# Kernel tuning notes

Measured on AMD Instinct MI355X. Metric: run time of the kernel, lower is better.

Reference implementation:

```python
import jax, jax.numpy as jnp
import numpy as np

H = 256        # hidden_dim == num_features
C = 10         # num_classes
N = 100000     # nodes
E = 1600000    # edges
BN_EPS = 1e-5
NEG_SLOPE = 0.1


def _bn(h, gamma, beta):
    # training-mode BatchNorm1d over node dim, biased variance (torch semantics)
    mu = jnp.mean(h, axis=0)
    var = jnp.mean(jnp.square(h - mu), axis=0)
    return (h - mu) * jax.lax.rsqrt(var + BN_EPS) * gamma + beta


def setup_inputs() -> dict:
    key = jax.random.key(0)
    ks = jax.random.split(key, 12)
    s = 1.0 / np.sqrt(H)
    x = jax.random.normal(ks[0], (N, H), dtype=jnp.float32)
    edge_index = jax.random.randint(ks[1], (2, E), 0, N, dtype=jnp.int64)
    return {
        "x": x,
        "edge_index": edge_index,
        # GIN MLP: lin1 -> bn -> relu -> lin2
        "W1": jax.random.uniform(ks[2], (H, H), jnp.float32, -s, s),
        "b1": jnp.zeros((H,), jnp.float32),
        "g_mlp": jnp.ones((H,), jnp.float32),
        "be_mlp": jnp.zeros((H,), jnp.float32),
        "W2": jax.random.uniform(ks[3], (H, H), jnp.float32, -s, s),
        "b2": jnp.zeros((H,), jnp.float32),
        # bn4
        "g4": jnp.ones((H,), jnp.float32),
        "be4": jnp.zeros((H,), jnp.float32),
        # head
        "Wl1": jax.random.uniform(ks[4], (H, H // 2), jnp.float32, -s, s),
        "bl1": jnp.zeros((H // 2,), jnp.float32),
        "Wl3": jax.random.uniform(ks[5], (H // 2, C), jnp.float32, -s, s),
        "bl3": jnp.zeros((C,), jnp.float32),
    }


def reference(x, edge_index, W1, b1, g_mlp, be_mlp, W2, b2, g4, be4, Wl1, bl1, Wl3, bl3):
    lrelu = lambda h: jax.nn.leaky_relu(h, NEG_SLOPE)
    src, dst = edge_index[0], edge_index[1]
    # GINConv: sum-aggregate neighbor messages (source_to_target), eps=0
    agg = jax.ops.segment_sum(x[src], dst, num_segments=x.shape[0])  # [N,H]
    h = agg + x  # (1+eps)*x + sum
    # PyG MLP([H,H,H]): lin -> batch_norm -> relu -> lin (plain last)
    h = jax.nn.relu(_bn(h @ W1 + b1, g_mlp, be_mlp)) @ W2 + b2
    x1 = lrelu(h)                     # relu(conv1(...), 0.1); dropout p=0
    h = lrelu(x1)                     # relu(x1, 0.1)
    h = lrelu(_bn(h, g4, be4))        # relu(bn4(x), 0.1); dropout p=0
    h = x + 0.01 * h                  # residual with original features
    h = lrelu(h @ Wl1 + bl1)
    return h @ Wl3 + bl3              # [N, C]
```

## Files before the change

kernel.cpp:

```cpp
#include <hip/hip_runtime.h>

constexpr int NN = 100000;
constexpr int NE = 1600000;
constexpr int NBUCK = 782;
constexpr int CGRID = 98;

typedef __attribute__((ext_vector_type(4))) float  f32x4;
typedef __attribute__((ext_vector_type(2))) float  f32x2;
typedef __attribute__((ext_vector_type(8))) short  bf16x8;

__device__ __forceinline__ float bf2f(unsigned short u) {
  union { unsigned int i; float f; } c;
  c.i = ((unsigned int)u) << 16;
  return c.f;
}
__device__ __forceinline__ short f2bf(float f) {
  union { float f; unsigned int i; } c; c.f = f;
  unsigned int i = c.i + 0x7fffu + ((c.i >> 16) & 1u);
  return (short)(i >> 16);
}
__device__ __forceinline__ unsigned char f2fp8(float f) {
  int w = __builtin_amdgcn_cvt_pk_fp8_f32(f, 0.f, 0, false);
  return (unsigned char)(w & 0xff);
}
__device__ __forceinline__ void up4(int wv, float* f) {
  f32x2 a = __builtin_amdgcn_cvt_pk_f32_fp8(wv, false);
  f32x2 b = __builtin_amdgcn_cvt_pk_f32_fp8(wv, true);
  f[0] = a[0]; f[1] = a[1]; f[2] = b[0]; f[3] = b[1];
}

__device__ __forceinline__ void gload16(const void* g, void* l) {
  __builtin_amdgcn_global_load_lds(
      (const __attribute__((address_space(1))) unsigned int*)g,
      (__attribute__((address_space(3))) unsigned int*)l, 16, 0, 0);
}

__global__ void k_detect(const int* __restrict__ ew, int* __restrict__ flag,
                         float* __restrict__ zst) {
  __shared__ int bad;
  if (threadIdx.x == 0) bad = 0;
  for (int i = threadIdx.x; i < 1024; i += 256) zst[i] = 0.f;
  __syncthreads();
  int nz = 0;
  for (int i = threadIdx.x; i < 2048; i += 256) nz |= ew[2 * i + 1];
  if (nz) atomicOr(&bad, 1);
  __syncthreads();
  if (threadIdx.x == 0) *flag = (bad == 0) ? 1 : 0;
}

__global__ void k_cvtW(const float* __restrict__ W1, const float* __restrict__ W2,
                       const float* __restrict__ Wl1, const float* __restrict__ Wl3,
                       unsigned char* __restrict__ W1T8, unsigned char* __restrict__ W2T8,
                       short* __restrict__ Wl1T, short* __restrict__ Wl3T) {
  int b = blockIdx.x, t = threadIdx.x;
  if (b < 256)       W1T8[b * 256 + t]       = f2fp8(W1[t * 256 + b]);
  else if (b < 512){ int n = b - 256; W2T8[n * 256 + t] = f2fp8(W2[t * 256 + n]); }
  else if (b < 640){ int n = b - 512; Wl1T[n * 256 + t] = f2bf(Wl1[t * 128 + n]); }
  else {
    if (t < 128) {
#pragma unroll
      for (int c = 0; c < 16; ++c)
        Wl3T[c * 128 + t] = (c < 10) ? f2bf(Wl3[t * 10 + c]) : (short)0;
    }
  }
}

__global__ void k_cvtX(const float* __restrict__ x, void* __restrict__ xq) {
  int c = blockIdx.x * 256 + threadIdx.x;
  float4 a = ((const float4*)x)[2 * (size_t)c];
  float4 b = ((const float4*)x)[2 * (size_t)c + 1];
  int p0 = 0, p1 = 0;
  p0 = __builtin_amdgcn_cvt_pk_fp8_f32(a.x, a.y, p0, false);
  p0 = __builtin_amdgcn_cvt_pk_fp8_f32(a.z, a.w, p0, true);
  p1 = __builtin_amdgcn_cvt_pk_fp8_f32(b.x, b.y, p1, false);
  p1 = __builtin_amdgcn_cvt_pk_fp8_f32(b.z, b.w, p1, true);
  ((int2*)xq)[c] = make_int2(p0, p1);
}

__global__ __launch_bounds__(1024) void k_count(const int* __restrict__ ew,
                                                const int* __restrict__ flag,
                                                int* __restrict__ cntmat) {
  __shared__ int lcnt[NBUCK];
  int m64 = *flag;
  int t = threadIdx.x;
  for (int i = t; i < NBUCK; i += 1024) lcnt[i] = 0;
  __syncthreads();
  int base = blockIdx.x * 16384;
#pragma unroll
  for (int u = 0; u < 16; u++) {
    int e = base + u * 1024 + t;
    if (e < NE) {
      int d = m64 ? ew[2 * (NE + e)] : ew[NE + e];
      atomicAdd(&lcnt[d >> 7], 1);
    }
  }
  __syncthreads();
  for (int i = t; i < NBUCK; i += 1024) cntmat[blockIdx.x * NBUCK + i] = lcnt[i];
}

__global__ __launch_bounds__(256) void k_cscan(int* __restrict__ cntmat,
                                               int* __restrict__ tot) {
  int wid = (blockIdx.x * 256 + threadIdx.x) >> 6;
  int lane = threadIdx.x & 63;
  if (wid >= NBUCK) return;
  int v0 = (lane < CGRID) ? cntmat[lane * NBUCK + wid] : 0;
  int v1 = (lane + 64 < CGRID) ? cntmat[(lane + 64) * NBUCK + wid] : 0;
  int s0 = v0;
#pragma unroll
  for (int o = 1; o < 64; o <<= 1) { int u = __shfl_up(s0, o); if (lane >= o) s0 += u; }
  int s1 = v1;
#pragma unroll
  for (int o = 1; o < 64; o <<= 1) { int u = __shfl_up(s1, o); if (lane >= o) s1 += u; }
  int t0 = __shfl(s0, 63);
  int t1 = __shfl(s1, 63);
  if (lane < CGRID) cntmat[lane * NBUCK + wid] = s0 - v0;
  if (lane + 64 < CGRID) cntmat[(lane + 64) * NBUCK + wid] = t0 + s1 - v1;
  if (lane == 0) tot[wid] = t0 + t1;
}

__global__ __launch_bounds__(1024) void k_bscan(const int* __restrict__ tot,
                                                int* __restrict__ bases,
                                                int* __restrict__ off_) {
  __shared__ int s[1024];
  int t = threadIdx.x;
  int v = (t < NBUCK) ? tot[t] : 0;
  s[t] = v; __syncthreads();
  for (int o = 1; o < 1024; o <<= 1) {
    int u = (t >= o) ? s[t - o] : 0;
    __syncthreads();
    s[t] += u;
    __syncthreads();
  }
  if (t < NBUCK) bases[t] = s[t] - v;
  if (t == 0) { bases[NBUCK] = NE; off_[NN] = NE; }
}

__global__ __launch_bounds__(1024) void k_scatter(const int* __restrict__ ew,
                                                  const int* __restrict__ flag,
                                                  const int* __restrict__ cntmat,
                                                  const int* __restrict__ bases,
                                                  int* __restrict__ pairs) {
  __shared__ int lcur[NBUCK];
  int m64 = *flag;
  int t = threadIdx.x;
  for (int i = t; i < NBUCK; i += 1024)
    lcur[i] = bases[i] + cntmat[blockIdx.x * NBUCK + i];
  __syncthreads();
  int base = blockIdx.x * 16384;
#pragma unroll
  for (int u = 0; u < 16; u++) {
    int e = base + u * 1024 + t;
    if (e < NE) {
      int d = m64 ? ew[2 * (NE + e)] : ew[NE + e];
      int s = m64 ? ew[2 * e] : ew[e];
      int slot = atomicAdd(&lcur[d >> 7], 1);
      pairs[slot] = s | ((d & 127) << 17);
    }
  }
}

__global__ __launch_bounds__(256) void k_bsort(const int* __restrict__ pairs,
                                               const int* __restrict__ bases,
                                               int* __restrict__ off_,
                                               int* __restrict__ csr) {
  __shared__ int lcnt[128], lofs[128], lcur[128];
  int b = blockIdx.x, t = threadIdx.x;
  int s0 = bases[b], s1 = bases[b + 1];
  if (t < 128) lcnt[t] = 0;
  __syncthreads();
  for (int j = s0 + t; j < s1; j += 256) atomicAdd(&lcnt[(pairs[j] >> 17) & 127], 1);
  __syncthreads();
  int v = (t < 128) ? lcnt[t] : 0;
  if (t < 128) lofs[t] = v;
  __syncthreads();
  for (int o = 1; o < 128; o <<= 1) {
    int u = (t >= o && t < 128) ? lofs[t - o] : 0;
    __syncthreads();
    if (t < 128) lofs[t] += u;
    __syncthreads();
  }
  if (t < 128) {
    int ex = lofs[t] - v;
    lcur[t] = ex;
    int node = b * 128 + t;
    if (node < NN) off_[node] = s0 + ex;
  }
  __syncthreads();
  for (int j = s0 + t; j < s1; j += 256) {
    int p = pairs[j];
    int slot = atomicAdd(&lcur[(p >> 17) & 127], 1);
    csr[s0 + slot] = p & 0x1FFFF;
  }
}

__global__ __launch_bounds__(256) void k_agg2(const void* __restrict__ xq,
                                              const int* __restrict__ off_,
                                              const int* __restrict__ csr,
                                              unsigned char* __restrict__ h0) {
  int node = blockIdx.x * 4 + (threadIdx.x >> 6);
  int lane = threadIdx.x & 63;
  const unsigned char* xb = (const unsigned char*)xq;
  size_t boff = (size_t)lane * 4;
  int s0 = off_[node], s1 = off_[node + 1];
  int sw = *(const int*)(xb + (size_t)node * 256 + boff);
  f32x2 slo = __builtin_amdgcn_cvt_pk_f32_fp8(sw, false);
  f32x2 shi = __builtin_amdgcn_cvt_pk_f32_fp8(sw, true);
  float a0 = slo[0], a1 = slo[1], a2 = shi[0], a3 = shi[1];
  int j = s0;
  while (j + 8 <= s1) {
    int idx[8];
#pragma unroll
    for (int u = 0; u < 8; u++) idx[u] = csr[j + u];
    int w[8];
#pragma unroll
    for (int u = 0; u < 8; u++) w[u] = *(const int*)(xb + (size_t)idx[u] * 256 + boff);
#pragma unroll
    for (int u = 0; u < 8; u++) {
      f32x2 lo = __builtin_amdgcn_cvt_pk_f32_fp8(w[u], false);
      f32x2 hi = __builtin_amdgcn_cvt_pk_f32_fp8(w[u], true);
      a0 += lo[0]; a1 += lo[1]; a2 += hi[0]; a3 += hi[1];
    }
    j += 8;
  }
  if (j + 4 <= s1) {
    int idx[4];
#pragma unroll
    for (int u = 0; u < 4; u++) idx[u] = csr[j + u];
    int w[4];
#pragma unroll
    for (int u = 0; u < 4; u++) w[u] = *(const int*)(xb + (size_t)idx[u] * 256 + boff);
#pragma unroll
    for (int u = 0; u < 4; u++) {
      f32x2 lo = __builtin_amdgcn_cvt_pk_f32_fp8(w[u], false);
      f32x2 hi = __builtin_amdgcn_cvt_pk_f32_fp8(w[u], true);
      a0 += lo[0]; a1 += lo[1]; a2 += hi[0]; a3 += hi[1];
    }
    j += 4;
  }
  for (; j < s1; j++) {
    int s = csr[j];
    int w = *(const int*)(xb + (size_t)s * 256 + boff);
    f32x2 lo = __builtin_amdgcn_cvt_pk_f32_fp8(w, false);
    f32x2 hi = __builtin_amdgcn_cvt_pk_f32_fp8(w, true);
    a0 += lo[0]; a1 += lo[1]; a2 += hi[0]; a3 += hi[1];
  }
  int o = 0;
  o = __builtin_amdgcn_cvt_pk_fp8_f32(a0, a1, o, false);
  o = __builtin_amdgcn_cvt_pk_fp8_f32(a2, a3, o, true);
  ((int*)h0)[(size_t)node * 64 + lane] = o;
}

template <int ACT, int TIN, int STATS>
__global__ __launch_bounds__(256, 2) void k_gemm8(
    const unsigned char* __restrict__ A, const unsigned char* __restrict__ BT,
    const float* __restrict__ bias, unsigned char* __restrict__ C, int M,
    const float* __restrict__ tsum, const float* __restrict__ tssq,
    const float* __restrict__ tg, const float* __restrict__ tbe,
    float* __restrict__ gsum, float* __restrict__ gssq) {
  __shared__ char smem[32768];
  __shared__ float lsc[256], lsh[256];
  __shared__ float lsum[128], lssq[128];
  int tid = threadIdx.x, lane = tid & 63, w = tid >> 6;
  if (TIN) {
    float mu = tsum[tid] / (float)M;
    float var = tssq[tid] / (float)M - mu * mu;
    float rs = rsqrtf(var + 1e-5f);
    float sc = tg[tid] * rs;
    lsc[tid] = sc; lsh[tid] = tbe[tid] - mu * sc;
  }
  if (STATS && tid < 128) { lsum[tid] = 0.f; lssq[tid] = 0.f; }
  int bm = blockIdx.x >> 1, bn = blockIdx.x & 1;
  int bm0 = bm * 128, bn0 = bn * 128;
  int wm = w >> 1, wn = w & 1;
  int lr = lane & 15, lg = lane >> 4;
  f32x4 acc[4][4] = {};
  __syncthreads();

  int4 stg[2];

#pragma unroll 1
  for (int it = 0; it < 4; ++it) {
    int b = it & 1;
    if (it == 0) {
      if (TIN) {
#pragma unroll
        for (int i = 0; i < 2; ++i) {
          int p = i * 256 + tid, unit = p >> 3, u = (p & 7) ^ (unit & 7);
          int srow = unit * 2 + (u >> 2), slot = u & 3;
          int grow = bm0 + srow; if (grow > M - 1) grow = M - 1;
          stg[i] = *(const int4*)(A + (size_t)grow * 256 + slot * 16);
        }
      } else {
#pragma unroll
        for (int q = 0; q < 2; ++q) {
          int wc = w * 2 + q;
          int p = wc * 64 + lane, unit = p >> 3, u = (p & 7) ^ (unit & 7);
          int srow = unit * 2 + (u >> 2), slot = u & 3;
          int grow = bm0 + srow; if (grow > M - 1) grow = M - 1;
          gload16(A + (size_t)grow * 256 + slot * 16, smem + wc * 1024);
        }
      }
#pragma unroll
      for (int q = 0; q < 2; ++q) {
        int wc = w * 2 + q;
        int p = wc * 64 + lane, unit = p >> 3, u = (p & 7) ^ (unit & 7);
        int srow = unit * 2 + (u >> 2), slot = u & 3;
        gload16(BT + (size_t)(bn0 + srow) * 256 + slot * 16, smem + 8192 + wc * 1024);
      }
      if (TIN) {
#pragma unroll
        for (int i = 0; i < 2; ++i) {
          int p = i * 256 + tid, unit = p >> 3, u = (p & 7) ^ (unit & 7);
          int slot = u & 3;
          int k0 = slot * 16;
          float f[16];
          up4(stg[i].x, f); up4(stg[i].y, f + 4); up4(stg[i].z, f + 8); up4(stg[i].w, f + 12);
#pragma unroll
          for (int jj = 0; jj < 16; ++jj) f[jj] = fmaxf(f[jj] * lsc[k0 + jj] + lsh[k0 + jj], 0.f);
          int w0 = 0, w1 = 0, w2 = 0, w3 = 0;
          w0 = __builtin_amdgcn_cvt_pk_fp8_f32(f[0], f[1], w0, false);
          w0 = __builtin_amdgcn_cvt_pk_fp8_f32(f[2], f[3], w0, true);
          w1 = __builtin_amdgcn_cvt_pk_fp8_f32(f[4], f[5], w1, false);
          w1 = __builtin_amdgcn_cvt_pk_fp8_f32(f[6], f[7], w1, true);
          w2 = __builtin_amdgcn_cvt_pk_fp8_f32(f[8], f[9], w2, false);
          w2 = __builtin_amdgcn_cvt_pk_fp8_f32(f[10], f[11], w2, true);
          w3 = __builtin_amdgcn_cvt_pk_fp8_f32(f[12], f[13], w3, false);
          w3 = __builtin_amdgcn_cvt_pk_fp8_f32(f[14], f[15], w3, true);
          *(int4*)(smem + p * 16) = make_int4(w0, w1, w2, w3);
        }
      }
      __syncthreads();
    }
    int ktn = (it + 1) * 64;
    if (it < 3) {
      char* nb = smem + (b ^ 1) * 16384;
      if (TIN) {
#pragma unroll
        for (int i = 0; i < 2; ++i) {
          int p = i * 256 + tid, unit = p >> 3, u = (p & 7) ^ (unit & 7);
          int srow = unit * 2 + (u >> 2), slot = u & 3;
          int grow = bm0 + srow; if (grow > M - 1) grow = M - 1;
          stg[i] = *(const int4*)(A + (size_t)grow * 256 + ktn + slot * 16);
        }
      } else {
#pragma unroll
        for (int q = 0; q < 2; ++q) {
          int wc = w * 2 + q;
          int p = wc * 64 + lane, unit = p >> 3, u = (p & 7) ^ (unit & 7);
          int srow = unit * 2 + (u >> 2), slot = u & 3;
          int grow = bm0 + srow; if (grow > M - 1) grow = M - 1;
          gload16(A + (size_t)grow * 256 + ktn + slot * 16, nb + wc * 1024);
        }
      }
#pragma unroll
      for (int q = 0; q < 2; ++q) {
        int wc = w * 2 + q;
        int p = wc * 64 + lane, unit = p >> 3, u = (p & 7) ^ (unit & 7);
        int srow = unit * 2 + (u >> 2), slot = u & 3;
        gload16(BT + (size_t)(bn0 + srow) * 256 + ktn + slot * 16, nb + 8192 + wc * 1024);
      }
    }
    const char* sa = smem + b * 16384;
    const char* sb = sa + 8192;
#pragma unroll
    for (int ks = 0; ks < 2; ++ks) {
      long af[4], bfr[4];
#pragma unroll
      for (int mi = 0; mi < 4; ++mi) {
        int row = wm * 64 + mi * 16 + lr;
        int unit = row >> 1;
        int u = ((row & 1) * 4 + ks * 2 + (lg >> 1)) ^ (unit & 7);
        af[mi] = *(const long*)(sa + unit * 128 + u * 16 + (lg & 1) * 8);
      }
#pragma unroll
      for (int ni = 0; ni < 4; ++ni) {
        int row = wn * 64 + ni * 16 + lr;
        int unit = row >> 1;
        int u = ((row & 1) * 4 + ks * 2 + (lg >> 1)) ^ (unit & 7);
        bfr[ni] = *(const long*)(sb + unit * 128 + u * 16 + (lg & 1) * 8);
      }
#pragma unroll
      for (int mi = 0; mi < 4; ++mi)
#pragma unroll
        for (int ni = 0; ni < 4; ++ni)
          acc[mi][ni] = __builtin_amdgcn_mfma_f32_16x16x32_fp8_fp8(af[mi], bfr[ni], acc[mi][ni], 0, 0, 0);
    }
    if (TIN && it < 3) {
      char* nb = smem + (b ^ 1) * 16384;
#pragma unroll
      for (int i = 0; i < 2; ++i) {
        int p = i * 256 + tid, unit = p >> 3, u = (p & 7) ^ (unit & 7);
        int slot = u & 3;
        int k0 = ktn + slot * 16;
        float f[16];
        up4(stg[i].x, f); up4(stg[i].y, f + 4); up4(stg[i].z, f + 8); up4(stg[i].w, f + 12);
#pragma unroll
        for (int jj = 0; jj < 16; ++jj) f[jj] = fmaxf(f[jj] * lsc[k0 + jj] + lsh[k0 + jj], 0.f);
        int w0 = 0, w1 = 0, w2 = 0, w3 = 0;
        w0 = __builtin_amdgcn_cvt_pk_fp8_f32(f[0], f[1], w0, false);
        w0 = __builtin_amdgcn_cvt_pk_fp8_f32(f[2], f[3], w0, true);
        w1 = __builtin_amdgcn_cvt_pk_fp8_f32(f[4], f[5], w1, false);
        w1 = __builtin_amdgcn_cvt_pk_fp8_f32(f[6], f[7], w1, true);
        w2 = __builtin_amdgcn_cvt_pk_fp8_f32(f[8], f[9], w2, false);
        w2 = __builtin_amdgcn_cvt_pk_fp8_f32(f[10], f[11], w2, true);
        w3 = __builtin_amdgcn_cvt_pk_fp8_f32(f[12], f[13], w3, false);
        w3 = __builtin_amdgcn_cvt_pk_fp8_f32(f[14], f[15], w3, true);
        *(int4*)(nb + p * 16) = make_int4(w0, w1, w2, w3);
      }
    }
    __syncthreads();
  }

  unsigned char* zs = (unsigned char*)smem;
#pragma unroll
  for (int ni = 0; ni < 4; ++ni) {
    int col = wn * 64 + ni * 16 + lr;
    float bv = bias[bn0 + col];
    float ps = 0.f, pq = 0.f;
#pragma unroll
    for (int mi = 0; mi < 4; ++mi) {
#pragma unroll
      for (int r = 0; r < 4; ++r) {
        int row = wm * 64 + mi * 16 + lg * 4 + r;
        float tv = acc[mi][ni][r] + bv;
        if (ACT == 1) tv = tv > 0.f ? tv : 0.01f * tv;
        if (STATS && (bm0 + row) < M) { ps += tv; pq += tv * tv; }
        zs[row * 144 + col] = f2fp8(tv);
      }
    }
    if (STATS) {
      ps += __shfl_xor(ps, 16); pq += __shfl_xor(pq, 16);
      ps += __shfl_xor(ps, 32); pq += __shfl_xor(pq, 32);
      if (lane < 16) {
        atomicAdd(&lsum[wn * 64 + ni * 16 + lane], ps);
        atomicAdd(&lssq[wn * 64 + ni * 16 + lane], pq);
      }
    }
  }
  __syncthreads();
  {
    int row = tid >> 1;
    int grow = bm0 + row;
    if (grow < M) {
#pragma unroll
      for (int i = 0; i < 4; ++i) {
        int cs = (tid & 1) * 64 + i * 16;
        int4 v = *(const int4*)(zs + row * 144 + cs);
        *(int4*)(C + (size_t)grow * 256 + bn0 + cs) = v;
      }
    }
  }
  if (STATS) {
    if (tid < 128) {
      atomicAdd(&gsum[bn0 + tid], lsum[tid]);
      atomicAdd(&gssq[bn0 + tid], lssq[tid]);
    }
  }
}

__global__ __launch_bounds__(256, 2) void k_head(const unsigned char* __restrict__ Vq,
                                                 const float* __restrict__ x,
                                                 const short* __restrict__ BT,
                                                 const float* __restrict__ bl1,
                                                 const short* __restrict__ wl3t,
                                                 const float* __restrict__ bl3,
                                                 const float* __restrict__ tsum,
                                                 const float* __restrict__ tssq,
                                                 const float* __restrict__ tg,
                                                 const float* __restrict__ tbe,
                                                 float* __restrict__ out, int M) {
  __shared__ char smem[65536];
  __shared__ float lsc[256], lsh[256];
  __shared__ short wl3s[2048];
  int tid = threadIdx.x;
  int lane = tid & 63, w = tid >> 6;
  {
    float mu = tsum[tid] / (float)M;
    float var = tssq[tid] / (float)M - mu * mu;
    float rs = rsqrtf(var + 1e-5f);
    float sc = tg[tid] * rs;
    lsc[tid] = sc; lsh[tid] = tbe[tid] - mu * sc;
  }
  {
    int p = w * 64 + lane;
    gload16(wl3t + (size_t)p * 8, (char*)wl3s + w * 1024);
  }
  int bm0 = blockIdx.x * 128;
  int wm = w >> 1, wn = w & 1;
  int lr = lane & 15, lg = lane >> 4;
  f32x4 acc[4][4] = {};
  __syncthreads();

  int2 stgv[4];
  float stgx[4][8];

#pragma unroll 1
  for (int it = 0; it < 4; ++it) {
    int b = it & 1;
    if (it == 0) {
#pragma unroll
      for (int i = 0; i < 4; ++i) {
        int p = tid + 256 * i, row = p >> 3, s = (p & 7) ^ (row & 7);
        int grow = bm0 + row; if (grow > M - 1) grow = M - 1;
        size_t base = (size_t)grow * 256 + s * 8;
        stgv[i] = *(const int2*)(Vq + base);
        *(float4*)&stgx[i][0] = *(const float4*)(x + base);
        *(float4*)&stgx[i][4] = *(const float4*)(x + base + 4);
      }
#pragma unroll
      for (int q = 0; q < 4; ++q) {
        int wc = w * 4 + q;
        int p = wc * 64 + lane, row = p >> 3, s = (p & 7) ^ (row & 7);
        gload16(BT + (size_t)row * 256 + s * 8, smem + 16384 + wc * 1024);
      }
#pragma unroll
      for (int i = 0; i < 4; ++i) {
        int p = tid + 256 * i, row = p >> 3, s = (p & 7) ^ (row & 7);
        int k0 = s * 8;
        float fv[8];
        up4(stgv[i].x, fv); up4(stgv[i].y, fv + 4);
        bf16x8 o;
#pragma unroll
        for (int jj = 0; jj < 8; ++jj) {
          float f = fv[jj] * lsc[k0 + jj] + lsh[k0 + jj];
          f = f > 0.f ? f : 0.1f * f;
          o[jj] = f2bf(stgx[i][jj] + 0.01f * f);
        }
        *(bf16x8*)(smem + p * 16) = o;
      }
      __syncthreads();
    }
    int ktn = (it + 1) * 64;
    if (it < 3) {
      char* nb = smem + (b ^ 1) * 32768;
#pragma unroll
      for (int i = 0; i < 4; ++i) {
        int p = tid + 256 * i, row = p >> 3, s = (p & 7) ^ (row & 7);
        int grow = bm0 + row; if (grow > M - 1) grow = M - 1;
        size_t base = (size_t)grow * 256 + ktn + s * 8;
        stgv[i] = *(const int2*)(Vq + base);
        *(float4*)&stgx[i][0] = *(const float4*)(x + base);
        *(float4*)&stgx[i][4] = *(const float4*)(x + base + 4);
      }
#pragma unroll
      for (int q = 0; q < 4; ++q) {
        int wc = w * 4 + q;
        int p = wc * 64 + lane, row = p >> 3, s = (p & 7) ^ (row & 7);
        gload16(BT + (size_t)row * 256 + ktn + s * 8, nb + 16384 + wc * 1024);
      }
    }
    const char* sa = smem + b * 32768;
    const char* sb = sa + 16384;
#pragma unroll
    for (int ks = 0; ks < 2; ++ks) {
      bf16x8 af[4], bfr[4];
#pragma unroll
      for (int mi = 0; mi < 4; ++mi) {
        int row = wm * 64 + mi * 16 + lr;
        int q = (lg + 4 * ks) ^ (row & 7);
        af[mi] = *(const bf16x8*)(sa + row * 128 + q * 16);
      }
#pragma unroll
      for (int ni = 0; ni < 4; ++ni) {
        int row = wn * 64 + ni * 16 + lr;
        int q = (lg + 4 * ks) ^ (row & 7);
        bfr[ni] = *(const bf16x8*)(sb + row * 128 + q * 16);
      }
#pragma unroll
      for (int mi = 0; mi < 4; ++mi)
#pragma unroll
        for (int ni = 0; ni < 4; ++ni)
          acc[mi][ni] = __builtin_amdgcn_mfma_f32_16x16x32_bf16(af[mi], bfr[ni], acc[mi][ni], 0, 0, 0);
    }
    if (it < 3) {
      char* nb = smem + (b ^ 1) * 32768;
#pragma unroll
      for (int i = 0; i < 4; ++i) {
        int p = tid + 256 * i, row = p >> 3, s = (p & 7) ^ (row & 7);
        int k0 = ktn + s * 8;
        float fv[8];
        up4(stgv[i].x, fv); up4(stgv[i].y, fv + 4);
        bf16x8 o;
#pragma unroll
        for (int jj = 0; jj < 8; ++jj) {
          float f = fv[jj] * lsc[k0 + jj] + lsh[k0 + jj];
          f = f > 0.f ? f : 0.1f * f;
          o[jj] = f2bf(stgx[i][jj] + 0.01f * f);
        }
        *(bf16x8*)(nb + p * 16) = o;
      }
    }
    __syncthreads();
  }

  short* zs = (short*)smem;
#pragma unroll
  for (int ni = 0; ni < 4; ++ni) {
    int col = wn * 64 + ni * 16 + lr;
    float bv = bl1[col];
#pragma unroll
    for (int mi = 0; mi < 4; ++mi) {
#pragma unroll
      for (int r = 0; r < 4; ++r) {
        int row = wm * 64 + mi * 16 + lg * 4 + r;
        float tv = acc[mi][ni][r] + bv;
        tv = tv > 0.f ? tv : 0.1f * tv;
        zs[row * 136 + col] = f2bf(tv);
      }
    }
  }
  __syncthreads();

  f32x4 acc2[2] = {};
#pragma unroll
  for (int kk = 0; kk < 4; ++kk) {
    bf16x8 bfr = *(const bf16x8*)((const char*)wl3s + lr * 256 + (kk * 4 + lg) * 16);
#pragma unroll
    for (int m = 0; m < 2; ++m) {
      int row = (w * 2 + m) * 16 + lr;
      bf16x8 af = *(const bf16x8*)((const char*)zs + row * 272 + (kk * 4 + lg) * 16);
      acc2[m] = __builtin_amdgcn_mfma_f32_16x16x32_bf16(af, bfr, acc2[m], 0, 0, 0);
    }
  }
  if (lr < 10) {
    float bv = bl3[lr];
#pragma unroll
    for (int m = 0; m < 2; ++m) {
#pragma unroll
      for (int r = 0; r < 4; ++r) {
        int row = (w * 2 + m) * 16 + lg * 4 + r;
        int grow = bm0 + row;
        if (grow < M) out[(size_t)grow * 10 + lr] = acc2[m][r] + bv;
      }
    }
  }
}

extern "C" void kernel_launch(void* const* d_in, const int* in_sizes, int n_in,
                              void* d_out, int out_size, void* d_ws, size_t ws_size,
                              hipStream_t stream) {
  const float* x   = (const float*)d_in[0];
  const int*   ew  = (const int*)d_in[1];
  const float* W1  = (const float*)d_in[2];
  const float* b1  = (const float*)d_in[3];
  const float* g1  = (const float*)d_in[4];
  const float* be1 = (const float*)d_in[5];
  const float* W2  = (const float*)d_in[6];
  const float* b2  = (const float*)d_in[7];
  const float* g4  = (const float*)d_in[8];
  const float* be4 = (const float*)d_in[9];
  const float* Wl1 = (const float*)d_in[10];
  const float* bl1 = (const float*)d_in[11];
  const float* Wl3 = (const float*)d_in[12];
  const float* bl3 = (const float*)d_in[13];
  float* out = (float*)d_out;

  char* ws = (char*)d_ws;
  const size_t OFF_OFF  = 0;
  const size_t OFF_BASES= 400128;
  const size_t OFF_CNT  = 800256;
  const size_t OFF_WL3T = 1106944;
  const size_t OFF_TOT  = 1114112;
  const size_t OFF_STATS= 1200384;
  const size_t OFF_FLAG = 1208576;
  const size_t OFF_W1T  = 1209216;
  const size_t OFF_W2T  = 1340288;
  const size_t OFF_WL1T = 1471360;
  const size_t OFF_CSR  = 1536896;
  const size_t OFF_BUFA = 7936896;
  const size_t OFF_BUFB = 59136896;
  if (ws_size < 110336896) return;

  int* off_  = (int*)(ws + OFF_OFF);
  int* bases_= (int*)(ws + OFF_BASES);
  int* cnt_  = (int*)(ws + OFF_CNT);
  int* tot_  = (int*)(ws + OFF_TOT);
  float* sum1 = (float*)(ws + OFF_STATS);
  float* ssq1 = sum1 + 256;
  float* sum4 = sum1 + 512;
  float* ssq4 = sum1 + 768;
  int* flag_ = (int*)(ws + OFF_FLAG);
  unsigned char* W1T8 = (unsigned char*)(ws + OFF_W1T);
  unsigned char* W2T8 = (unsigned char*)(ws + OFF_W2T);
  short* Wl1T = (short*)(ws + OFF_WL1T);
  short* Wl3T = (short*)(ws + OFF_WL3T);
  int* csr_   = (int*)(ws + OFF_CSR);
  unsigned char* bufA = (unsigned char*)(ws + OFF_BUFA);
  unsigned char* bufB = (unsigned char*)(ws + OFF_BUFB);
  int* pairs_ = (int*)(ws + OFF_BUFA);
  void* xq    = (void*)bufB;

  k_detect<<<1, 256, 0, stream>>>(ew, flag_, sum1);
  k_cvtW<<<641, 256, 0, stream>>>(W1, W2, Wl1, Wl3, W1T8, W2T8, Wl1T, Wl3T);
  k_cvtX<<<12500, 256, 0, stream>>>(x, xq);
  k_count<<<CGRID, 1024, 0, stream>>>(ew, flag_, cnt_);
  k_cscan<<<196, 256, 0, stream>>>(cnt_, tot_);
  k_bscan<<<1, 1024, 0, stream>>>(tot_, bases_, off_);
  k_scatter<<<CGRID, 1024, 0, stream>>>(ew, flag_, cnt_, bases_, pairs_);
  k_bsort<<<NBUCK, 256, 0, stream>>>(pairs_, bases_, off_, csr_);
  k_agg2<<<25000, 256, 0, stream>>>(xq, off_, csr_, bufA);
  k_gemm8<0, 0, 1><<<1564, 256, 0, stream>>>(bufA, W1T8, b1, bufB, NN,
                                             nullptr, nullptr, nullptr, nullptr,
                                             sum1, ssq1);
  k_gemm8<1, 1, 1><<<1564, 256, 0, stream>>>(bufB, W2T8, b2, bufA, NN,
                                             sum1, ssq1, g1, be1, sum4, ssq4);
  k_head<<<782, 256, 0, stream>>>(bufA, x, Wl1T, bl1, Wl3T, bl3,
                                  sum4, ssq4, g4, be4, out, NN);
}
```

Measured before the change: 257.6 us.

## Merge detect, weight convert, x convert and edge count into one phase kernel

Four independent preprocessing kernels (int64 detection, weight transpose/convert, x fp8 conversion, destination bucket counting) are combined into one launch that picks its role from the block index. Each block that needs the int64 flag now recomputes it locally instead of reading a flag from a separate kernel. This removes three kernel launches and their serialization gaps, and lets the small jobs overlap with the large x conversion. In exchange the edge-layout check is done redundantly in every count and scatter block, and the 1024-thread blocks may change occupancy for the conversion part.

```diff
diff --git a/kernel.cpp b/kernel.cpp
--- a/kernel.cpp
+++ b/kernel.cpp
@@ -4,6 +4,9 @@
 constexpr int NE = 1600000;
 constexpr int NBUCK = 782;
 constexpr int CGRID = 98;
+constexpr int PH_CVTX = 3125;
+constexpr int PH_CNT_END = PH_CVTX + CGRID;
+constexpr int PH_GRID = PH_CNT_END + 161;
 
 typedef __attribute__((ext_vector_type(4))) float  f32x4;
 typedef __attribute__((ext_vector_type(2))) float  f32x2;
@@ -35,67 +38,65 @@
       (__attribute__((address_space(3))) unsigned int*)l, 16, 0, 0);
 }
 
-__global__ void k_detect(const int* __restrict__ ew, int* __restrict__ flag,
-                         float* __restrict__ zst) {
-  __shared__ int bad;
-  if (threadIdx.x == 0) bad = 0;
-  for (int i = threadIdx.x; i < 1024; i += 256) zst[i] = 0.f;
-  __syncthreads();
-  int nz = 0;
-  for (int i = threadIdx.x; i < 2048; i += 256) nz |= ew[2 * i + 1];
-  if (nz) atomicOr(&bad, 1);
-  __syncthreads();
-  if (threadIdx.x == 0) *flag = (bad == 0) ? 1 : 0;
-}
-
-__global__ void k_cvtW(const float* __restrict__ W1, const float* __restrict__ W2,
-                       const float* __restrict__ Wl1, const float* __restrict__ Wl3,
-                       unsigned char* __restrict__ W1T8, unsigned char* __restrict__ W2T8,
-                       short* __restrict__ Wl1T, short* __restrict__ Wl3T) {
-  int b = blockIdx.x, t = threadIdx.x;
-  if (b < 256)       W1T8[b * 256 + t]       = f2fp8(W1[t * 256 + b]);
-  else if (b < 512){ int n = b - 256; W2T8[n * 256 + t] = f2fp8(W2[t * 256 + n]); }
-  else if (b < 640){ int n = b - 512; Wl1T[n * 256 + t] = f2bf(Wl1[t * 128 + n]); }
-  else {
-    if (t < 128) {
-#pragma unroll
-      for (int c = 0; c < 16; ++c)
-        Wl3T[c * 128 + t] = (c < 10) ? f2bf(Wl3[t * 10 + c]) : (short)0;
-    }
-  }
-}
-
-__global__ void k_cvtX(const float* __restrict__ x, void* __restrict__ xq) {
-  int c = blockIdx.x * 256 + threadIdx.x;
-  float4 a = ((const float4*)x)[2 * (size_t)c];
-  float4 b = ((const float4*)x)[2 * (size_t)c + 1];
-  int p0 = 0, p1 = 0;
-  p0 = __builtin_amdgcn_cvt_pk_fp8_f32(a.x, a.y, p0, false);
-  p0 = __builtin_amdgcn_cvt_pk_fp8_f32(a.z, a.w, p0, true);
-  p1 = __builtin_amdgcn_cvt_pk_fp8_f32(b.x, b.y, p1, false);
-  p1 = __builtin_amdgcn_cvt_pk_fp8_f32(b.z, b.w, p1, true);
-  ((int2*)xq)[c] = make_int2(p0, p1);
-}
-
-__global__ __launch_bounds__(1024) void k_count(const int* __restrict__ ew,
-                                                const int* __restrict__ flag,
-                                                int* __restrict__ cntmat) {
+__global__ __launch_bounds__(1024) void k_phase1(
+    const float* __restrict__ x, void* __restrict__ xq,
+    const int* __restrict__ ew, int* __restrict__ cntmat,
+    const float* __restrict__ W1, const float* __restrict__ W2,
+    const float* __restrict__ Wl1, const float* __restrict__ Wl3,
+    unsigned char* __restrict__ W1T8, unsigned char* __restrict__ W2T8,
+    short* __restrict__ Wl1T, short* __restrict__ Wl3T,
+    float* __restrict__ zst) {
   __shared__ int lcnt[NBUCK];
-  int m64 = *flag;
-  int t = threadIdx.x;
-  for (int i = t; i < NBUCK; i += 1024) lcnt[i] = 0;
-  __syncthreads();
-  int base = blockIdx.x * 16384;
-#pragma unroll
-  for (int u = 0; u < 16; u++) {
-    int e = base + u * 1024 + t;
-    if (e < NE) {
-      int d = m64 ? ew[2 * (NE + e)] : ew[NE + e];
-      atomicAdd(&lcnt[d >> 7], 1);
-    }
-  }
-  __syncthreads();
-  for (int i = t; i < NBUCK; i += 1024) cntmat[blockIdx.x * NBUCK + i] = lcnt[i];
+  __shared__ int badsh;
+  int bid = blockIdx.x, tid = threadIdx.x;
+  if (bid < PH_CVTX) {
+    int c = bid * 1024 + tid;
+    float4 a = ((const float4*)x)[2 * (size_t)c];
+    float4 b = ((const float4*)x)[2 * (size_t)c + 1];
+    int p0 = 0, p1 = 0;
+    p0 = __builtin_amdgcn_cvt_pk_fp8_f32(a.x, a.y, p0, false);
+    p0 = __builtin_amdgcn_cvt_pk_fp8_f32(a.z, a.w, p0, true);
+    p1 = __builtin_amdgcn_cvt_pk_fp8_f32(b.x, b.y, p1, false);
+    p1 = __builtin_amdgcn_cvt_pk_fp8_f32(b.z, b.w, p1, true);
+    ((int2*)xq)[c] = make_int2(p0, p1);
+  } else if (bid < PH_CNT_END) {
+    int cb = bid - PH_CVTX;
+    if (tid == 0) badsh = 0;
+    for (int i = tid; i < NBUCK; i += 1024) lcnt[i] = 0;
+    __syncthreads();
+    int nz = 0;
+    for (int i = tid; i < 2048; i += 1024) nz |= ew[2 * i + 1];
+    if (nz) atomicOr(&badsh, 1);
+    __syncthreads();
+    int m64 = (badsh == 0);
+    int base = cb * 16384;
+#pragma unroll
+    for (int u = 0; u < 16; u++) {
+      int e = base + u * 1024 + tid;
+      if (e < NE) {
+        int d = m64 ? ew[2 * (NE + e)] : ew[NE + e];
+        atomicAdd(&lcnt[d >> 7], 1);
+      }
+    }
+    __syncthreads();
+    for (int i = tid; i < NBUCK; i += 1024) cntmat[cb * NBUCK + i] = lcnt[i];
+  } else {
+    int wb = bid - PH_CNT_END;
+    if (wb == 0) zst[tid] = 0.f;
+    int b = wb * 4 + (tid >> 8), t = tid & 255;
+    if (b < 641) {
+      if (b < 256)       W1T8[b * 256 + t]       = f2fp8(W1[t * 256 + b]);
+      else if (b < 512){ int n = b - 256; W2T8[n * 256 + t] = f2fp8(W2[t * 256 + n]); }
+      else if (b < 640){ int n = b - 512; Wl1T[n * 256 + t] = f2bf(Wl1[t * 128 + n]); }
+      else {
+        if (t < 128) {
+#pragma unroll
+          for (int c = 0; c < 16; ++c)
+            Wl3T[c * 128 + t] = (c < 10) ? f2bf(Wl3[t * 10 + c]) : (short)0;
+        }
+      }
+    }
+  }
 }
 
 __global__ __launch_bounds__(256) void k_cscan(int* __restrict__ cntmat,
@@ -136,16 +137,21 @@
 }
 
 __global__ __launch_bounds__(1024) void k_scatter(const int* __restrict__ ew,
-                                                  const int* __restrict__ flag,
                                                   const int* __restrict__ cntmat,
                                                   const int* __restrict__ bases,
                                                   int* __restrict__ pairs) {
   __shared__ int lcur[NBUCK];
-  int m64 = *flag;
+  __shared__ int badsh;
   int t = threadIdx.x;
+  if (t == 0) badsh = 0;
   for (int i = t; i < NBUCK; i += 1024)
     lcur[i] = bases[i] + cntmat[blockIdx.x * NBUCK + i];
   __syncthreads();
+  int nz = 0;
+  for (int i = t; i < 2048; i += 1024) nz |= ew[2 * i + 1];
+  if (nz) atomicOr(&badsh, 1);
+  __syncthreads();
+  int m64 = (badsh == 0);
   int base = blockIdx.x * 16384;
 #pragma unroll
   for (int u = 0; u < 16; u++) {
@@ -662,7 +668,6 @@
   const size_t OFF_WL3T = 1106944;
   const size_t OFF_TOT  = 1114112;
   const size_t OFF_STATS= 1200384;
-  const size_t OFF_FLAG = 1208576;
   const size_t OFF_W1T  = 1209216;
   const size_t OFF_W2T  = 1340288;
   const size_t OFF_WL1T = 1471360;
@@ -679,7 +684,6 @@
   float* ssq1 = sum1 + 256;
   float* sum4 = sum1 + 512;
   float* ssq4 = sum1 + 768;
-  int* flag_ = (int*)(ws + OFF_FLAG);
   unsigned char* W1T8 = (unsigned char*)(ws + OFF_W1T);
   unsigned char* W2T8 = (unsigned char*)(ws + OFF_W2T);
   short* Wl1T = (short*)(ws + OFF_WL1T);
@@ -690,13 +694,11 @@
   int* pairs_ = (int*)(ws + OFF_BUFA);
   void* xq    = (void*)bufB;
 
-  k_detect<<<1, 256, 0, stream>>>(ew, flag_, sum1);
-  k_cvtW<<<641, 256, 0, stream>>>(W1, W2, Wl1, Wl3, W1T8, W2T8, Wl1T, Wl3T);
-  k_cvtX<<<12500, 256, 0, stream>>>(x, xq);
-  k_count<<<CGRID, 1024, 0, stream>>>(ew, flag_, cnt_);
+  k_phase1<<<PH_GRID, 1024, 0, stream>>>(x, xq, ew, cnt_, W1, W2, Wl1, Wl3,
+                                         W1T8, W2T8, Wl1T, Wl3T, sum1);
   k_cscan<<<196, 256, 0, stream>>>(cnt_, tot_);
   k_bscan<<<1, 1024, 0, stream>>>(tot_, bases_, off_);
-  k_scatter<<<CGRID, 1024, 0, stream>>>(ew, flag_, cnt_, bases_, pairs_);
+  k_scatter<<<CGRID, 1024, 0, stream>>>(ew, cnt_, bases_, pairs_);
   k_bsort<<<NBUCK, 256, 0, stream>>>(pairs_, bases_, off_, csr_);
   k_agg2<<<25000, 256, 0, stream>>>(xq, off_, csr_, bufA);
   k_gemm8<0, 0, 1><<<1564, 256, 0, stream>>>(bufA, W1T8, b1, bufB, NN,
```

New measurement: 248.9 us. -3.4%, faster.
